# Kernel optimization log

Measured on AMD Instinct MI355X. Metric: run time of the kernel, lower is better.

Reference implementation:

```python
import jax, jax.numpy as jnp
import numpy as np

N, E, D, G, NTYPES = 50000, 400000, 64, 512, 64


def _bn(x, g, b):
    # BatchNorm1d in training mode: biased batch stats, eps=1e-5, affine g/b
    mu = x.mean(0)
    var = ((x - mu) ** 2).mean(0)
    return g * (x - mu) * jax.lax.rsqrt(var + 1e-5) + b


def _rotmat(a):
    t, p, q = a[0], a[1], a[2]
    ct, st = jnp.cos(t), jnp.sin(t)
    cp, sp = jnp.cos(p), jnp.sin(p)
    cq, sq = jnp.cos(q), jnp.sin(q)
    z = jnp.zeros(())
    o = jnp.ones(())
    Rt = jnp.array([[ct, -st, z], [st, ct, z], [z, z, o]])
    Rp = jnp.array([[cp, z, -sp], [z, o, z], [sp, z, cp]])
    Rq = jnp.array([[o, z, z], [z, cq, -sq], [z, sq, cq]])
    return Rt @ Rp @ Rq


def _egat(src, dst, nf, ef, Wnode, bnode, Wni, Wnj, Wfij, attn, H):
    # DGL EGATConv: edge feats from src/dst node + edge projections, edge-softmax attention over dst
    n = nf.shape[0]
    f_out = jax.nn.leaky_relu((nf @ Wni)[src] + (nf @ Wnj)[dst] + ef @ Wfij)  # [E, H*D]
    f_out = f_out.reshape(-1, H, D)
    e = (f_out * attn[None]).sum(-1)  # [E, H]
    emax = jax.ops.segment_max(e, dst, num_segments=n)
    ee = jnp.exp(e - emax[dst])
    a = ee / jax.ops.segment_sum(ee, dst, num_segments=n)[dst]
    hsrc = (nf @ Wnode + bnode).reshape(n, H, D)[src]
    h_out = jax.ops.segment_sum(hsrc * a[:, :, None], dst, num_segments=n)  # [N, H, D]
    return h_out, f_out


def _layer(src, dst, nh, eh, p, H, last):
    Wnode, bnode, Wni, Wnj, Wfij, attn, bnn_g, bnn_b, bne_g, bne_b, Wpn, bpn, Wpe, bpe = p
    hn, he = _egat(src, dst, nh, eh, Wnode, bnode, Wni, Wnj, Wfij, attn, H)
    if last:
        hn, he = hn.mean(1), he.mean(1)
    else:
        hn, he = hn.reshape(hn.shape[0], -1), he.reshape(he.shape[0], -1)
    hn = _bn(hn, bnn_g, bnn_b)
    he = _bn(he, bne_g, bne_b)
    return hn @ Wpn + bpn + nh, he @ Wpe + bpe + eh


def setup_inputs():
    key = jax.random.key(0)
    kit = iter(jax.random.split(key, 64))

    def rn(shape, s=0.05):
        return jax.random.normal(next(kit), shape, dtype=jnp.float32) * s

    inp = {}
    inp["ntype"] = jax.random.randint(next(kit), (N, 1), 0, NTYPES)
    inp["src"] = jax.random.randint(next(kit), (E,), 0, N)
    inp["dst"] = jax.random.randint(next(kit), (E,), 0, N)
    inp["graph_ids"] = jnp.sort(jax.random.randint(next(kit), (N,), 0, G))
    inp["angles_rot"] = rn((3,), 1.0)
    inp["angles_ref"] = rn((3,), 1.0)
    inp["efeats"] = rn((E, 3), 1.0)
    inp["emb_table"] = rn((NTYPES, D))
    inp["enc_W"] = rn((D, D)); inp["enc_b"] = jnp.zeros((D,))
    inp["ee_W1"] = rn((3, D)); inp["ee_b1"] = jnp.zeros((D,))
    inp["ee_W2"] = rn((D, D)); inp["ee_b2"] = jnp.zeros((D,))
    for nm in ["enc_bn1", "enc_bn2", "ee_bn1", "ee_bn2"]:
        inp[nm + "_g"] = jnp.ones((D,)); inp[nm + "_b"] = jnp.zeros((D,))
    for l, H in [(0, 2), (1, 1)]:
        p = "l%d_" % l
        inp[p + "Wnode"] = rn((D, H * D)); inp[p + "bnode"] = jnp.zeros((H * D,))
        inp[p + "Wni"] = rn((D, H * D)); inp[p + "Wnj"] = rn((D, H * D)); inp[p + "Wfij"] = rn((D, H * D))
        inp[p + "attn"] = rn((H, D))
        inp[p + "bnn_g"] = jnp.ones((H * D,)); inp[p + "bnn_b"] = jnp.zeros((H * D,))
        inp[p + "bne_g"] = jnp.ones((H * D,)); inp[p + "bne_b"] = jnp.zeros((H * D,))
        inp[p + "Wpn"] = rn((H * D, D)); inp[p + "bpn"] = jnp.zeros((D,))
        inp[p + "Wpe"] = rn((H * D, D)); inp[p + "bpe"] = jnp.zeros((D,))
    inp["dec_W"] = rn((4, D, D)); inp["dec_b"] = jnp.zeros((4, D))
    inp["dec_bn_g"] = jnp.ones((4, D)); inp["dec_bn_b"] = jnp.zeros((4, D))
    inp["dec_prelu"] = jnp.full((4,), 0.25, dtype=jnp.float32)
    inp["dec_Wout"] = rn((D, 1)); inp["dec_bout"] = jnp.zeros((1,))
    return inp


def reference(efeats, emb_table, enc_bn1_g, enc_bn1_b, enc_W, enc_b, enc_bn2_g, enc_bn2_b, ee_W1, ee_b1, ee_bn1_g, ee_bn1_b, ee_W2, ee_b2, ee_bn2_g, ee_bn2_b, l0_Wnode, l0_bnode, l0_Wni, l0_Wnj, l0_Wfij, l0_attn, l0_bnn_g, l0_bnn_b, l0_bne_g, l0_bne_b, l0_Wpn, l0_bpn, l0_Wpe, l0_bpe, l1_Wnode, l1_bnode, l1_Wni, l1_Wnj, l1_Wfij, l1_attn, l1_bnn_g, l1_bnn_b, l1_bne_g, l1_bne_b, l1_Wpn, l1_bpn, l1_Wpe, l1_bpe, dec_W, dec_b, dec_bn_g, dec_bn_b, dec_prelu, dec_Wout, dec_bout, ntype, src, dst, graph_ids, angles_rot, angles_ref):
    # node encoder: Embedding -> BN -> ReLU -> Linear -> BN -> ReLU
    nh = emb_table[ntype[:, 0]]
    nh = jax.nn.relu(_bn(nh, enc_bn1_g, enc_bn1_b))
    nh = jax.nn.relu(_bn(nh @ enc_W + enc_b, enc_bn2_g, enc_bn2_b))

    def edge_enc(f):
        h = jax.nn.relu(_bn(f @ ee_W1 + ee_b1, ee_bn1_g, ee_bn1_b))
        return jax.nn.relu(_bn(h @ ee_W2 + ee_b2, ee_bn2_g, ee_bn2_b))

    # rotation matrices built from sampled angles; torch.tensor([...]) detaches -> stop_gradient
    R_rot = jax.lax.stop_gradient(_rotmat(angles_rot))
    R_ref = -jax.lax.stop_gradient(_rotmat(angles_ref))
    eh = edge_enc(efeats @ R_rot) + edge_enc(efeats @ R_ref)

    p0 = (l0_Wnode, l0_bnode, l0_Wni, l0_Wnj, l0_Wfij, l0_attn, l0_bnn_g, l0_bnn_b, l0_bne_g, l0_bne_b, l0_Wpn, l0_bpn, l0_Wpe, l0_bpe)
    p1 = (l1_Wnode, l1_bnode, l1_Wni, l1_Wnj, l1_Wfij, l1_attn, l1_bnn_g, l1_bnn_b, l1_bne_g, l1_bne_b, l1_Wpn, l1_bpn, l1_Wpe, l1_bpe)
    nh, eh = _layer(src, dst, nh, eh, p0, 2, False)
    h1 = nh
    nh, eh = _layer(src, dst, nh, eh, p1, 1, True)
    h2 = nh

    h = nh
    for i in range(4):
        h = _bn(h @ dec_W[i] + dec_b[i], dec_bn_g[i], dec_bn_b[i])
        h = jnp.where(h >= 0.0, h, dec_prelu[i] * h)
    h = h @ dec_Wout + dec_bout
    # dgl.sum_nodes: per-graph sum over batched graphs
    return (h1, h2, jax.ops.segment_sum(h, graph_ids, num_segments=G))
```

## Files before the change

kernel.cpp:

```cpp
#include <hip/hip_runtime.h>
#include <math.h>

#define NN 50000
#define NE 400000
#define NG 512
#define EPS 1e-5f
#define NSLOT 256

typedef unsigned int u32;
typedef unsigned short u16;

typedef __attribute__((ext_vector_type(8))) short s16x8;
typedef __attribute__((ext_vector_type(4))) float f32x4;

__device__ __forceinline__ float b2f(u16 h) { return __uint_as_float(((u32)h) << 16); }
__device__ __forceinline__ u16 f2b(float f) {
    u32 x = __float_as_uint(f);
    u32 r = x + 0x7fffu + ((x >> 16) & 1u);
    return (u16)(r >> 16);
}
struct alignas(16) U16x8 { u16 s[8]; };
struct alignas(8) U16x4 { u16 s[4]; };
struct alignas(4) U16x2 { u16 s[2]; };

__device__ __forceinline__ void f4add(float4& a, const float4 b) {
    a.x += b.x; a.y += b.y; a.z += b.z; a.w += b.w;
}

__global__ void setup_kernel(const float* __restrict__ ang_rot, const float* __restrict__ ang_ref,
                             const float* __restrict__ W1, float* __restrict__ RWrot,
                             float* __restrict__ RWref) {
    int c = threadIdx.x;
    for (int which = 0; which < 2; ++which) {
        const float* a = which ? ang_ref : ang_rot;
        float t = a[0], p = a[1], q = a[2];
        float ct = cosf(t), st = sinf(t);
        float cp = cosf(p), sp = sinf(p);
        float cq = cosf(q), sq = sinf(q);
        float Rt[3][3] = {{ct, -st, 0.f}, {st, ct, 0.f}, {0.f, 0.f, 1.f}};
        float Rp[3][3] = {{cp, 0.f, -sp}, {0.f, 1.f, 0.f}, {sp, 0.f, cp}};
        float Rq[3][3] = {{1.f, 0.f, 0.f}, {0.f, cq, -sq}, {0.f, sq, cq}};
        float Rtp[3][3], R[3][3];
        for (int i = 0; i < 3; ++i)
            for (int j = 0; j < 3; ++j) {
                float s = 0.f;
                for (int k = 0; k < 3; ++k) s += Rt[i][k] * Rp[k][j];
                Rtp[i][j] = s;
            }
        for (int i = 0; i < 3; ++i)
            for (int j = 0; j < 3; ++j) {
                float s = 0.f;
                for (int k = 0; k < 3; ++k) s += Rtp[i][k] * Rq[k][j];
                R[i][j] = s;
            }
        float sgn = which ? -1.f : 1.f;
        float* RW = which ? RWref : RWrot;
        if (c < 64) {
            for (int j = 0; j < 3; ++j) {
                float s = 0.f;
                for (int m = 0; m < 3; ++m) s += sgn * R[j][m] * W1[m * 64 + c];
                RW[j * 64 + c] = s;
            }
        }
    }
}

#define NWT 17
struct WtJobs {
    const float* W[NWT];
    u16* WT[NWT];
    int K[NWT];
    int C[NWT];
};
__global__ __launch_bounds__(256) void wt_all_kernel(WtJobs jobs) {
    int job = blockIdx.x >> 5;
    int idx = ((blockIdx.x & 31) << 8) + threadIdx.x;
    int K = jobs.K[job], C = jobs.C[job];
    if (idx >= K * C) return;
    int k = idx / C, c = idx - k * C;
    jobs.WT[job][c * K + k] = f2b(jobs.W[job][idx]);
}

__global__ __launch_bounds__(256) void hist_kernel(const int* __restrict__ dst, int E,
                                                   int* __restrict__ deg) {
    int e = blockIdx.x * 256 + threadIdx.x;
    if (e < E) atomicAdd(&deg[dst[e]], 1);
}

__global__ __launch_bounds__(256) void scan_part_kernel(const int* __restrict__ deg,
                                                        int* __restrict__ bsum, int n) {
    int i = blockIdx.x * 256 + threadIdx.x;
    int v = (i < n) ? deg[i] : 0;
#pragma unroll
    for (int off = 1; off < 64; off <<= 1) v += __shfl_xor(v, off, 64);
    __shared__ int ws[4];
    if ((threadIdx.x & 63) == 0) ws[threadIdx.x >> 6] = v;
    __syncthreads();
    if (threadIdx.x == 0) bsum[blockIdx.x] = ws[0] + ws[1] + ws[2] + ws[3];
}

__global__ __launch_bounds__(256) void scan_top_kernel(int* __restrict__ bsum, int nb,
                                                       int* __restrict__ rowptr, int n,
                                                       int total) {
    __shared__ int s[256];
    int tid = threadIdx.x;
    s[tid] = (tid < nb) ? bsum[tid] : 0;
    __syncthreads();
    for (int off = 1; off < 256; off <<= 1) {
        int v = (tid >= off) ? s[tid - off] : 0;
        __syncthreads();
        s[tid] += v;
        __syncthreads();
    }
    if (tid < nb) bsum[tid] = (tid == 0) ? 0 : s[tid - 1];
    if (tid == 0) rowptr[n] = total;
}

__global__ __launch_bounds__(256) void scan_fill_kernel(const int* __restrict__ deg,
                                                        const int* __restrict__ bsum,
                                                        int* __restrict__ rowptr,
                                                        int* __restrict__ curs, int n) {
    __shared__ int s[256];
    int tid = threadIdx.x;
    int i = blockIdx.x * 256 + tid;
    int v = (i < n) ? deg[i] : 0;
    s[tid] = v;
    __syncthreads();
    for (int off = 1; off < 256; off <<= 1) {
        int t = (tid >= off) ? s[tid - off] : 0;
        __syncthreads();
        s[tid] += t;
        __syncthreads();
    }
    if (i < n) {
        int excl = s[tid] - v + bsum[blockIdx.x];
        rowptr[i] = excl;
        curs[i] = excl;
    }
}

__global__ __launch_bounds__(256) void fill_kernel(const int* __restrict__ src,
                                                   const int* __restrict__ dst,
                                                   const float* __restrict__ ef, int E,
                                                   int* __restrict__ curs,
                                                   int* __restrict__ esrc,
                                                   int* __restrict__ dsts,
                                                   float* __restrict__ efp) {
    int e = blockIdx.x * 256 + threadIdx.x;
    if (e >= E) return;
    int d = dst[e];
    int pos = atomicAdd(&curs[d], 1);
    esrc[pos] = src[e];
    dsts[pos] = d;
    efp[(long)pos * 3 + 0] = ef[(long)e * 3 + 0];
    efp[(long)pos * 3 + 1] = ef[(long)e * 3 + 1];
    efp[(long)pos * 3 + 2] = ef[(long)e * 3 + 2];
}

__global__ __launch_bounds__(256) void gather_emb_kernel(const int* __restrict__ ntype,
                                                         const float* __restrict__ emb,
                                                         u16* __restrict__ out, int n) {
    long i = (long)blockIdx.x * 256 + threadIdx.x;
    long e = i >> 3;
    if (e >= n) return;
    int c0 = (int)(i & 7) * 8;
    int t = ntype[e];
    float4 a = *(const float4*)&emb[(long)t * 64 + c0];
    float4 b = *(const float4*)&emb[(long)t * 64 + c0 + 4];
    U16x8 o;
    o.s[0] = f2b(a.x); o.s[1] = f2b(a.y); o.s[2] = f2b(a.z); o.s[3] = f2b(a.w);
    o.s[4] = f2b(b.x); o.s[5] = f2b(b.y); o.s[6] = f2b(b.z); o.s[7] = f2b(b.w);
    *(U16x8*)&out[e * 64 + c0] = o;
}

__global__ __launch_bounds__(256) void efstats_kernel(const float* __restrict__ ef, int E,
                                                      float* __restrict__ raw) {
    int tid = threadIdx.x;
    float a[9];
#pragma unroll
    for (int j = 0; j < 9; ++j) a[j] = 0.f;
    for (long e = (long)blockIdx.x * 256 + tid; e < E; e += (long)gridDim.x * 256) {
        float f0 = ef[e * 3 + 0], f1 = ef[e * 3 + 1], f2 = ef[e * 3 + 2];
        a[0] += f0; a[1] += f1; a[2] += f2;
        a[3] += f0 * f0; a[4] += f1 * f1; a[5] += f2 * f2;
        a[6] += f0 * f1; a[7] += f0 * f2; a[8] += f1 * f2;
    }
#pragma unroll
    for (int off = 1; off < 64; off <<= 1)
#pragma unroll
        for (int j = 0; j < 9; ++j) a[j] += __shfl_xor(a[j], off, 64);
    __shared__ float sred[4][9];
    int wv = tid >> 6, ln = tid & 63;
    if (ln == 0)
#pragma unroll
        for (int j = 0; j < 9; ++j) sred[wv][j] = a[j];
    __syncthreads();
    if (tid < 9) {
        float v = sred[0][tid] + sred[1][tid] + sred[2][tid] + sred[3][tid];
        atomicAdd(&raw[(size_t)(blockIdx.x & (NSLOT - 1)) * 16 + tid], v);
    }
}

__global__ void ee_stats_kernel(const float* __restrict__ efraw, const float* __restrict__ RWrot,
                                const float* __restrict__ RWref, const float* __restrict__ b1,
                                float* __restrict__ S_rot, float* __restrict__ S_ref, int E) {
    __shared__ float m[9];
    int t = threadIdx.x;
    if (t < 9) {
        float s = 0.f;
        for (int r = 0; r < NSLOT; ++r) s += efraw[r * 16 + t];
        m[t] = s;
    }
    __syncthreads();
    int br = t >> 6, c = t & 63;
    const float* RW = br ? RWref : RWrot;
    float* S = br ? S_ref : S_rot;
    float w0 = RW[c], w1 = RW[64 + c], w2 = RW[128 + c];
    float bb = b1[c];
    float mw = m[0] * w0 + m[1] * w1 + m[2] * w2;
    float sum = mw + (float)E * bb;
    float quad = m[3] * w0 * w0 + m[4] * w1 * w1 + m[5] * w2 * w2 +
                 2.f * (m[6] * w0 * w1 + m[7] * w0 * w2 + m[8] * w1 * w2);
    float ss = quad + 2.f * bb * mw + (float)E * bb * bb;
    S[c] = sum;
    S[64 + c] = ss;
}

template <int COLS>
__global__ __launch_bounds__(256) void colstats_kernel(const u16* __restrict__ xv, int rows,
                                                       float* __restrict__ raw) {
    constexpr int TPR = COLS / 8;
    constexpr int RPB = 256 / TPR;
    __shared__ float4 sA[256], sB[256], sC[256], sD[256];
    int tid = threadIdx.x;
    int c8 = tid % TPR;
    int rl = tid / TPR;
    float s[8], q[8];
#pragma unroll
    for (int j = 0; j < 8; ++j) { s[j] = 0.f; q[j] = 0.f; }
    const long stride = (long)gridDim.x * RPB;
    for (long r = (long)blockIdx.x * RPB + rl; r < rows; r += stride) {
        U16x8 t = *(const U16x8*)&xv[r * COLS + c8 * 8];
#pragma unroll
        for (int j = 0; j < 8; ++j) {
            float v = b2f(t.s[j]);
            s[j] += v;
            q[j] += v * v;
        }
    }
    sA[tid] = make_float4(s[0], s[1], s[2], s[3]);
    sB[tid] = make_float4(s[4], s[5], s[6], s[7]);
    sC[tid] = make_float4(q[0], q[1], q[2], q[3]);
    sD[tid] = make_float4(q[4], q[5], q[6], q[7]);
    __syncthreads();
    for (int off = 128; off >= TPR; off >>= 1) {
        if (tid < off) {
            f4add(sA[tid], sA[tid + off]); f4add(sB[tid], sB[tid + off]);
            f4add(sC[tid], sC[tid + off]); f4add(sD[tid], sD[tid + off]);
        }
        __syncthreads();
    }
    if (tid < TPR) {
        float* slot = raw + (size_t)(blockIdx.x & (NSLOT - 1)) * 256;
        int c = tid * 8;
        float4 a = sA[tid], b = sB[tid], cq = sC[tid], d = sD[tid];
        atomicAdd(&slot[c + 0], a.x); atomicAdd(&slot[c + 1], a.y);
        atomicAdd(&slot[c + 2], a.z); atomicAdd(&slot[c + 3], a.w);
        atomicAdd(&slot[c + 4], b.x); atomicAdd(&slot[c + 5], b.y);
        atomicAdd(&slot[c + 6], b.z); atomicAdd(&slot[c + 7], b.w);
        atomicAdd(&slot[COLS + c + 0], cq.x); atomicAdd(&slot[COLS + c + 1], cq.y);
        atomicAdd(&slot[COLS + c + 2], cq.z); atomicAdd(&slot[COLS + c + 3], cq.w);
        atomicAdd(&slot[COLS + c + 4], d.x); atomicAdd(&slot[COLS + c + 5], d.y);
        atomicAdd(&slot[COLS + c + 6], d.z); atomicAdd(&slot[COLS + c + 7], d.w);
    }
}

__global__ __launch_bounds__(256) void finalize_stats_kernel(const float* __restrict__ raw,
                                                             float* __restrict__ stats, int n) {
    int i = threadIdx.x;
    if (i >= n) return;
    float s = 0.f;
    for (int r = 0; r < NSLOT; ++r) s += raw[r * 256 + i];
    stats[i] = s;
}

__global__ __launch_bounds__(256) void bn_act_kernel(const u16* __restrict__ x,
                                                     u16* __restrict__ y, long rows, int cols,
                                                     const float* __restrict__ acc,
                                                     const float* __restrict__ g,
                                                     const float* __restrict__ b,
                                                     float inv_rows) {
    long i = (long)blockIdx.x * 256 + threadIdx.x;
    long total8 = rows * (long)cols / 8;
    if (i >= total8) return;
    long base = i * 8;
    int c0 = (int)(base % cols);
    U16x8 xv = *(const U16x8*)&x[base];
    U16x8 o;
#pragma unroll
    for (int j = 0; j < 8; ++j) {
        int c = c0 + j;
        float mu = acc[c] * inv_rows;
        float var = acc[cols + c] * inv_rows - mu * mu;
        float al = g[c] * rsqrtf(fmaxf(var, 0.f) + EPS);
        float be = b[c] - mu * al;
        o.s[j] = f2b(fmaxf(al * b2f(xv.s[j]) + be, 0.f));
    }
    *(U16x8*)&y[base] = o;
}


template <int K, int COLS, bool XBF, bool RBF, bool OBF, bool SOUT>
__global__ __launch_bounds__(256) void mfma_mm_kernel(
    const void* __restrict__ Xv, const u16* __restrict__ WT, const float* __restrict__ bias,
    const void* __restrict__ resv, void* __restrict__ Yv, int rows, int preop,
    const float* __restrict__ stats, const float* __restrict__ g, const float* __restrict__ b,
    float inv_rows, const float* __restrict__ prelu, int prelu_idx, float* __restrict__ raw) {
    constexpr int NCT = COLS / 16;
    constexpr int NKK = K / 32;
    __shared__ float al[K], be[K];
    __shared__ float ssum[SOUT ? COLS : 1], ssq[SOUT ? COLS : 1];
    const int tid = threadIdx.x;
    if (preop) {
        for (int k = tid; k < K; k += 256) {
            float mu = stats[k] * inv_rows;
            float var = stats[K + k] * inv_rows - mu * mu;
            float a = g[k] * rsqrtf(fmaxf(var, 0.f) + EPS);
            al[k] = a;
            be[k] = b[k] - mu * a;
        }
    }
    if (SOUT) {
        for (int i = tid; i < COLS; i += 256) { ssum[i] = 0.f; ssq[i] = 0.f; }
    }
    __syncthreads();
    const int lane = tid & 63, wv = tid >> 6;
    const int q = lane >> 4, rr = lane & 15;
    const long r0 = ((long)blockIdx.x * 4 + wv) * 16;
    const bool act = r0 < rows;
    const float pa = (preop == 3) ? prelu[prelu_idx] : 0.f;
    s16x8 afr[NKK];
    if (act) {
#pragma unroll
        for (int kk = 0; kk < NKK; ++kk) {
            float v[8];
            if (XBF) {
                U16x8 t = *(const U16x8*)((const u16*)Xv + (r0 + rr) * K + kk * 32 + q * 8);
#pragma unroll
                for (int j = 0; j < 8; ++j) v[j] = b2f(t.s[j]);
            } else {
                const float* xp = (const float*)Xv + (r0 + rr) * K + kk * 32 + q * 8;
                float4 t0 = *(const float4*)xp;
                float4 t1 = *(const float4*)(xp + 4);
                v[0] = t0.x; v[1] = t0.y; v[2] = t0.z; v[3] = t0.w;
                v[4] = t1.x; v[5] = t1.y; v[6] = t1.z; v[7] = t1.w;
            }
            union { u16 u[8]; s16x8 s; } o;
#pragma unroll
            for (int j = 0; j < 8; ++j) {
                float xx = v[j];
                if (preop) {
                    int k = kk * 32 + q * 8 + j;
                    xx = al[k] * xx + be[k];
                    if (preop == 2) xx = fmaxf(xx, 0.f);
                    else if (preop == 3) xx = (xx >= 0.f) ? xx : pa * xx;
                }
                o.u[j] = f2b(xx);
            }
            afr[kk] = o.s;
        }
#pragma unroll
        for (int ct = 0; ct < NCT; ++ct) {
            f32x4 acc = (f32x4){0.f, 0.f, 0.f, 0.f};
#pragma unroll
            for (int kk = 0; kk < NKK; ++kk) {
                s16x8 bfr = *(const s16x8*)&WT[(size_t)(ct * 16 + rr) * K + kk * 32 + q * 8];
                acc = __builtin_amdgcn_mfma_f32_16x16x32_bf16(afr[kk], bfr, acc, 0, 0, 0);
            }
            int col = ct * 16 + rr;
            float bb = bias ? bias[col] : 0.f;
            float fs = 0.f, fq = 0.f;
#pragma unroll
            for (int r = 0; r < 4; ++r) {
                long orr = r0 + q * 4 + r;
                float vv = acc[r] + bb;
                if (resv) {
                    if (RBF) vv += b2f(((const u16*)resv)[orr * COLS + col]);
                    else vv += ((const float*)resv)[orr * COLS + col];
                }
                if (OBF) ((u16*)Yv)[orr * COLS + col] = f2b(vv);
                else ((float*)Yv)[orr * COLS + col] = vv;
                if (SOUT) { fs += vv; fq += vv * vv; }
            }
            if (SOUT) {
                fs += __shfl_xor(fs, 16, 64); fs += __shfl_xor(fs, 32, 64);
                fq += __shfl_xor(fq, 16, 64); fq += __shfl_xor(fq, 32, 64);
                if (q == 0) {
                    atomicAdd(&ssum[col], fs);
                    atomicAdd(&ssq[col], fq);
                }
            }
        }
    }
    if (SOUT) {
        __syncthreads();
        float* slot = raw + (size_t)(blockIdx.x & (NSLOT - 1)) * 256;
        for (int i = tid; i < COLS; i += 256) {
            atomicAdd(&slot[i], ssum[i]);
            atomicAdd(&slot[COLS + i], ssq[i]);
        }
    }
}

template <int COLS, bool XBF>
__global__ __launch_bounds__(256) void mfma_mm3_kernel(
    const void* __restrict__ Xv, const u16* __restrict__ WT0, const u16* __restrict__ WT1,
    const u16* __restrict__ WT2, const float* __restrict__ bias2, u16* __restrict__ Y0,
    u16* __restrict__ Y1, u16* __restrict__ Y2, int rows) {
    constexpr int NCT = COLS / 16;
    const int tid = threadIdx.x;
    const int lane = tid & 63, wv = tid >> 6;
    const int q = lane >> 4, rr = lane & 15;
    const long r0 = ((long)blockIdx.x * 4 + wv) * 16;
    if (r0 >= rows) return;
    s16x8 afr[2];
#pragma unroll
    for (int kk = 0; kk < 2; ++kk) {
        if (XBF) {
            afr[kk] = *(const s16x8*)((const u16*)Xv + (r0 + rr) * 64 + kk * 32 + q * 8);
        } else {
            const float* xp = (const float*)Xv + (r0 + rr) * 64 + kk * 32 + q * 8;
            float4 t0 = *(const float4*)xp;
            float4 t1 = *(const float4*)(xp + 4);
            union { u16 u[8]; s16x8 s; } o;
            o.u[0] = f2b(t0.x); o.u[1] = f2b(t0.y); o.u[2] = f2b(t0.z); o.u[3] = f2b(t0.w);
            o.u[4] = f2b(t1.x); o.u[5] = f2b(t1.y); o.u[6] = f2b(t1.z); o.u[7] = f2b(t1.w);
            afr[kk] = o.s;
        }
    }
    const u16* wts[3] = {WT0, WT1, WT2};
    u16* ys[3] = {Y0, Y1, Y2};
#pragma unroll
    for (int m = 0; m < 3; ++m) {
#pragma unroll
        for (int ct = 0; ct < NCT; ++ct) {
            f32x4 acc = (f32x4){0.f, 0.f, 0.f, 0.f};
#pragma unroll
            for (int kk = 0; kk < 2; ++kk) {
                s16x8 bfr = *(const s16x8*)&wts[m][(size_t)(ct * 16 + rr) * 64 + kk * 32 + q * 8];
                acc = __builtin_amdgcn_mfma_f32_16x16x32_bf16(afr[kk], bfr, acc, 0, 0, 0);
            }
            int col = ct * 16 + rr;
            float bb = (m == 2) ? bias2[col] : 0.f;
#pragma unroll
            for (int r = 0; r < 4; ++r) {
                long orr = r0 + q * 4 + r;
                ys[m][orr * COLS + col] = f2b(acc[r] + bb);
            }
        }
    }
}

template <bool STORE>
__global__ __launch_bounds__(256) void mfma_ee2_kernel(
    const float* __restrict__ efp, const float* __restrict__ RWrot,
    const float* __restrict__ RWref, const float* __restrict__ b1v, const u16* __restrict__ W2T,
    const float* __restrict__ b2, const float* __restrict__ S1r, const float* __restrict__ S1f,
    const float* __restrict__ S2r, const float* __restrict__ S2f, const float* __restrict__ g1,
    const float* __restrict__ bn1b, const float* __restrict__ g2, const float* __restrict__ bn2b,
    u16* __restrict__ EH, int E, float inv_rows, float* __restrict__ rawA,
    float* __restrict__ rawB) {
    constexpr int ESTR = 72;
    __shared__ float rws[2][192];
    __shared__ float al1[2][64], be1[2][64];
    __shared__ float al2[2][64], be2[2][64];
    __shared__ float ssum[2][64], ssq[2][64];
    __shared__ u16 ets[STORE ? 64 * ESTR : 1];
    const int tid = threadIdx.x;
    if (tid < 192) {
        rws[0][tid] = RWrot[tid];
        rws[1][tid] = RWref[tid];
    }
    if (tid < 128) {
        int br = tid >> 6, k = tid & 63;
        const float* S1 = br ? S1f : S1r;
        float mu = S1[k] * inv_rows;
        float var = S1[64 + k] * inv_rows - mu * mu;
        float a = g1[k] * rsqrtf(fmaxf(var, 0.f) + EPS);
        al1[br][k] = a;
        be1[br][k] = bn1b[k] - mu * a + a * b1v[k];
        if (STORE) {
            const float* S2 = br ? S2f : S2r;
            mu = S2[k] * inv_rows;
            var = S2[64 + k] * inv_rows - mu * mu;
            a = g2[k] * rsqrtf(fmaxf(var, 0.f) + EPS);
            al2[br][k] = a;
            be2[br][k] = bn2b[k] - mu * a + a * b2[k];
        } else {
            ssum[br][k] = 0.f;
            ssq[br][k] = 0.f;
        }
    }
    __syncthreads();
    const int lane = tid & 63, wv = tid >> 6;
    const int q = lane >> 4, rr = lane & 15;
    const long r0 = ((long)blockIdx.x * 4 + wv) * 16;
    const long ar = r0 + rr;
    float e0 = efp[ar * 3], e1 = efp[ar * 3 + 1], e2 = efp[ar * 3 + 2];
    float v0[4][4];
#pragma unroll
    for (int br = 0; br < 2; ++br) {
        s16x8 afr[2];
#pragma unroll
        for (int kk = 0; kk < 2; ++kk) {
            union { u16 u[8]; s16x8 v; } t;
#pragma unroll
            for (int j = 0; j < 8; ++j) {
                int k = kk * 32 + q * 8 + j;
                float tv = e0 * rws[br][k] + e1 * rws[br][64 + k] + e2 * rws[br][128 + k];
                t.u[j] = f2b(fmaxf(al1[br][k] * tv + be1[br][k], 0.f));
            }
            afr[kk] = t.v;
        }
#pragma unroll
        for (int ct = 0; ct < 4; ++ct) {
            f32x4 acc = (f32x4){0.f, 0.f, 0.f, 0.f};
#pragma unroll
            for (int kk = 0; kk < 2; ++kk) {
                s16x8 bfr = *(const s16x8*)&W2T[(size_t)(ct * 16 + rr) * 64 + kk * 32 + q * 8];
                acc = __builtin_amdgcn_mfma_f32_16x16x32_bf16(afr[kk], bfr, acc, 0, 0, 0);
            }
            int col = ct * 16 + rr;
            if (STORE) {
#pragma unroll
                for (int r = 0; r < 4; ++r) {
                    float v = fmaxf(al2[br][col] * acc[r] + be2[br][col], 0.f);
                    if (br == 0) {
                        v0[ct][r] = v;
                    } else {
                        ets[(wv * 16 + q * 4 + r) * ESTR + col] = f2b(v0[ct][r] + v);
                    }
                }
            } else {
                float bb = b2[col];
                float s = 0.f, qq = 0.f;
#pragma unroll
                for (int r = 0; r < 4; ++r) {
                    float v = acc[r] + bb;
                    s += v;
                    qq += v * v;
                }
                s += __shfl_xor(s, 16, 64); s += __shfl_xor(s, 32, 64);
                qq += __shfl_xor(qq, 16, 64); qq += __shfl_xor(qq, 32, 64);
                if (q == 0) {
                    atomicAdd(&ssum[br][col], s);
                    atomicAdd(&ssq[br][col], qq);
                }
            }
        }
    }
    __syncthreads();
    if (STORE) {
        const long rb = (long)blockIdx.x * 64;
        for (int i = tid; i < 64 * 8; i += 256) {
            int row = i >> 3, c8 = i & 7;
            U16x8 v = *(const U16x8*)&ets[row * ESTR + c8 * 8];
            *(U16x8*)&EH[(rb + row) * 64 + c8 * 8] = v;
        }
    } else {
        if (tid < 128) {
            int br = tid >> 6, k = tid & 63;
            float* slot = (br ? rawB : rawA) + (size_t)(blockIdx.x & (NSLOT - 1)) * 256;
            atomicAdd(&slot[k], ssum[br][k]);
            atomicAdd(&slot[64 + k], ssq[br][k]);
        }
    }
}

template <int COLS, bool WRITE_F, bool SOUT>
__global__ __launch_bounds__(256) void mfma_egat_kernel(
    const u16* __restrict__ EH, const u16* __restrict__ WT, const u16* __restrict__ NI,
    const u16* __restrict__ NJ, const int* __restrict__ srcs, const int* __restrict__ dsts,
    const float* __restrict__ attn, u16* __restrict__ Fout, float* __restrict__ eatt, int E,
    float* __restrict__ raw) {
    constexpr int H = COLS / 64;
    constexpr int NCT = COLS / 16;
    constexpr int FSTR = COLS + 8;
    __shared__ float ssum[SOUT ? COLS : 1];
    __shared__ float ssq[SOUT ? COLS : 1];
    __shared__ u16 fts[WRITE_F ? 64 * FSTR : 1];
    const int tid = threadIdx.x;
    if (SOUT) {
        for (int i = tid; i < COLS; i += 256) { ssum[i] = 0.f; ssq[i] = 0.f; }
        __syncthreads();
    }
    const int lane = tid & 63, wv = tid >> 6;
    const int q = lane >> 4, rr = lane & 15;
    const long r0 = ((long)blockIdx.x * 4 + wv) * 16;
    s16x8 afr[2];
#pragma unroll
    for (int kk = 0; kk < 2; ++kk)
        afr[kk] = *(const s16x8*)&EH[(r0 + rr) * 64 + kk * 32 + q * 8];
    int sidx[4], didx[4];
#pragma unroll
    for (int r = 0; r < 4; ++r) {
        long orr = r0 + q * 4 + r;
        sidx[r] = srcs[orr];
        didx[r] = dsts[orr];
    }
    f32x4 acc[NCT];
#pragma unroll
    for (int ct = 0; ct < NCT; ++ct) {
        acc[ct] = (f32x4){0.f, 0.f, 0.f, 0.f};
#pragma unroll
        for (int kk = 0; kk < 2; ++kk) {
            s16x8 bfr = *(const s16x8*)&WT[(size_t)(ct * 16 + rr) * 64 + kk * 32 + q * 8];
            acc[ct] = __builtin_amdgcn_mfma_f32_16x16x32_bf16(afr[kk], bfr, acc[ct], 0, 0, 0);
        }
    }
    float part[H][4];
#pragma unroll
    for (int h = 0; h < H; ++h)
#pragma unroll
        for (int r = 0; r < 4; ++r) part[h][r] = 0.f;
#pragma unroll
    for (int ct = 0; ct < NCT; ++ct) {
        int col = ct * 16 + rr;
        float av = attn[col];
        const int h = (H == 2) ? (ct >> 2) : 0;
        float fs = 0.f, fq = 0.f;
#pragma unroll
        for (int r = 0; r < 4; ++r) {
            float f = acc[ct][r] + b2f(NI[(size_t)sidx[r] * COLS + col]) +
                      b2f(NJ[(size_t)didx[r] * COLS + col]);
            f = (f >= 0.f) ? f : 0.01f * f;
            if (WRITE_F) fts[(wv * 16 + q * 4 + r) * FSTR + col] = f2b(f);
            part[h][r] += f * av;
            if (SOUT) { fs += f; fq += f * f; }
        }
        if (SOUT) {
            fs += __shfl_xor(fs, 16, 64); fs += __shfl_xor(fs, 32, 64);
            fq += __shfl_xor(fq, 16, 64); fq += __shfl_xor(fq, 32, 64);
            if (q == 0) {
                atomicAdd(&ssum[col], fs);
                atomicAdd(&ssq[col], fq);
            }
        }
    }
#pragma unroll
    for (int h = 0; h < H; ++h)
#pragma unroll
        for (int r = 0; r < 4; ++r) {
            float p = part[h][r];
            p += __shfl_xor(p, 1, 64);
            p += __shfl_xor(p, 2, 64);
            p += __shfl_xor(p, 4, 64);
            p += __shfl_xor(p, 8, 64);
            part[h][r] = p;
        }
    if (rr == 0) {
#pragma unroll
        for (int r = 0; r < 4; ++r) {
            long pos = r0 + q * 4 + r;
            if (H == 2) {
                eatt[pos * 2 + 0] = part[0][r];
                eatt[pos * 2 + 1] = part[1][r];
            } else {
                eatt[pos] = part[0][r];
            }
        }
    }
    if (WRITE_F) {
        __syncthreads();
        const long rb = (long)blockIdx.x * 64;
        constexpr int CH = COLS / 8;
        for (int i = tid; i < 64 * CH; i += 256) {
            int row = i / CH, c8 = i % CH;
            U16x8 v = *(const U16x8*)&fts[row * FSTR + c8 * 8];
            *(U16x8*)&Fout[(rb + row) * COLS + c8 * 8] = v;
        }
    }
    if (SOUT) {
        __syncthreads();
        float* slot = raw + (size_t)(blockIdx.x & (NSLOT - 1)) * 256;
        for (int i = tid; i < COLS; i += 256) {
            atomicAdd(&slot[i], ssum[i]);
            atomicAdd(&slot[COLS + i], ssq[i]);
        }
    }
}

__global__ __launch_bounds__(256) void mfma_pe_kernel(
    const u16* __restrict__ X, const u16* __restrict__ WT, const float* __restrict__ bias,
    u16* __restrict__ EHio, int E, const float* __restrict__ stats, const float* __restrict__ g,
    const float* __restrict__ b, float inv_rows) {
    __shared__ float al[128], be[128];
    const int tid = threadIdx.x;
    if (tid < 128) {
        float mu = stats[tid] * inv_rows;
        float var = stats[128 + tid] * inv_rows - mu * mu;
        float a = g[tid] * rsqrtf(fmaxf(var, 0.f) + EPS);
        al[tid] = a;
        be[tid] = b[tid] - mu * a;
    }
    __syncthreads();
    const int lane = tid & 63, wv = tid >> 6;
    const int q = lane >> 4, rr = lane & 15;
    const long r0 = ((long)blockIdx.x * 4 + wv) * 16;
    s16x8 afr[4];
#pragma unroll
    for (int kk = 0; kk < 4; ++kk) {
        U16x8 t = *(const U16x8*)&X[(r0 + rr) * 128 + kk * 32 + q * 8];
        union { u16 u[8]; s16x8 v; } o;
#pragma unroll
        for (int j = 0; j < 8; ++j) {
            int k = kk * 32 + q * 8 + j;
            o.u[j] = f2b(al[k] * b2f(t.s[j]) + be[k]);
        }
        afr[kk] = o.v;
    }
#pragma unroll
    for (int ct = 0; ct < 4; ++ct) {
        f32x4 acc = (f32x4){0.f, 0.f, 0.f, 0.f};
#pragma unroll
        for (int kk = 0; kk < 4; ++kk) {
            s16x8 bfr = *(const s16x8*)&WT[(size_t)(ct * 16 + rr) * 128 + kk * 32 + q * 8];
            acc = __builtin_amdgcn_mfma_f32_16x16x32_bf16(afr[kk], bfr, acc, 0, 0, 0);
        }
        int col = ct * 16 + rr;
        float bb = bias[col];
#pragma unroll
        for (int r = 0; r < 4; ++r) {
            long orr = r0 + q * 4 + r;
            float v = acc[r] + bb + b2f(EHio[orr * 64 + col]);
            EHio[orr * 64 + col] = f2b(v);
        }
    }
}

template <int COLS, bool SOUT>
__global__ __launch_bounds__(256) void csr_aggregate_kernel(
    const int* __restrict__ rowptr, const int* __restrict__ esrc,
    const float* __restrict__ eatt, const u16* __restrict__ nodeh, float* __restrict__ hout,
    int n, float* __restrict__ raw) {
    constexpr int H = COLS / 64;
    constexpr int TPN = COLS / 2;
    constexpr int NPB = 256 / TPN;
    __shared__ float ssum[SOUT ? COLS : 1];
    __shared__ float ssq[SOUT ? COLS : 1];
    int tid = threadIdx.x;
    if (SOUT) {
        for (int i = tid; i < COLS; i += 256) { ssum[i] = 0.f; ssq[i] = 0.f; }
        __syncthreads();
    }
    int node = blockIdx.x * NPB + tid / TPN;
    bool act = node < n;
    int c = (tid % TPN) * 2;
    float a0 = 0.f, a1 = 0.f;
    if (act) {
        int h = (H == 2) ? (c >> 6) : 0;
        int p0 = rowptr[node], p1 = rowptr[node + 1];
        float m = -INFINITY, s = 0.f;
        for (int p = p0; p < p1; ++p) {
            float v = eatt[(long)p * H + h];
            float mn = fmaxf(m, v);
            s = s * expf(m - mn) + expf(v - mn);
            m = mn;
        }
        float inv = (s > 0.f) ? 1.f / s : 0.f;
        for (int p = p0; p < p1; ++p) {
            float w = expf(eatt[(long)p * H + h] - m) * inv;
            U16x2 v = *(const U16x2*)&nodeh[(long)esrc[p] * COLS + c];
            a0 += b2f(v.s[0]) * w;
            a1 += b2f(v.s[1]) * w;
        }
        *(float2*)&hout[(long)node * COLS + c] = make_float2(a0, a1);
    }
    if (SOUT) {
        if (act) {
            atomicAdd(&ssum[c], a0);
            atomicAdd(&ssum[c + 1], a1);
            atomicAdd(&ssq[c], a0 * a0);
            atomicAdd(&ssq[c + 1], a1 * a1);
        }
        __syncthreads();
        float* slot = raw + (size_t)(blockIdx.x & (NSLOT - 1)) * 256;
        for (int i = tid; i < COLS; i += 256) {
            atomicAdd(&slot[i], ssum[i]);
            atomicAdd(&slot[COLS + i], ssq[i]);
        }
    }
}

__global__ __launch_bounds__(256) void decoder_out_kernel(
    const u16* __restrict__ t3, const float* __restrict__ stats, const float* __restrict__ g,
    const float* __restrict__ b, const float* __restrict__ prelu, const float* __restrict__ Wout,
    const float* __restrict__ bout, const int* __restrict__ gid, float* __restrict__ pool,
    int rows, float inv_rows) {
    int tid = threadIdx.x;
    long r = (long)blockIdx.x * 4 + (tid >> 6);
    if (r >= rows) return;
    int k = tid & 63;
    float mu = stats[k] * inv_rows;
    float var = stats[64 + k] * inv_rows - mu * mu;
    float al = g[k] * rsqrtf(fmaxf(var, 0.f) + EPS);
    float be = b[k] - mu * al;
    float a = prelu[3];
    float v = al * b2f(t3[r * 64 + k]) + be;
    v = (v >= 0.f) ? v : a * v;
    v *= Wout[k];
#pragma unroll
    for (int off = 1; off < 64; off <<= 1) v += __shfl_xor(v, off, 64);
    if (k == 0) atomicAdd(&pool[gid[r]], v + bout[0]);
}

extern "C" void kernel_launch(void* const* d_in, const int* in_sizes, int n_in, void* d_out,
                              int out_size, void* d_ws, size_t ws_size, hipStream_t stream) {
    if (n_in < 57) return;
    const int* ntype = (const int*)d_in[0];
    const int* src = (const int*)d_in[1];
    const int* dst = (const int*)d_in[2];
    const int* gid = (const int*)d_in[3];
    const float* ang_rot = (const float*)d_in[4];
    const float* ang_ref = (const float*)d_in[5];
    const float* efeats = (const float*)d_in[6];
    const float* emb = (const float*)d_in[7];
    const float* enc_W = (const float*)d_in[8];
    const float* enc_b = (const float*)d_in[9];
    const float* ee_W1 = (const float*)d_in[10];
    const float* ee_b1 = (const float*)d_in[11];
    const float* ee_W2 = (const float*)d_in[12];
    const float* ee_b2 = (const float*)d_in[13];
    const float* enc_bn1_g = (const float*)d_in[14];
    const float* enc_bn1_b = (const float*)d_in[15];
    const float* enc_bn2_g = (const float*)d_in[16];
    const float* enc_bn2_b = (const float*)d_in[17];
    const float* ee_bn1_g = (const float*)d_in[18];
    const float* ee_bn1_b = (const float*)d_in[19];
    const float* ee_bn2_g = (const float*)d_in[20];
    const float* ee_bn2_b = (const float*)d_in[21];
    const float* l0_Wnode = (const float*)d_in[22];
    const float* l0_bnode = (const float*)d_in[23];
    const float* l0_Wni = (const float*)d_in[24];
    const float* l0_Wnj = (const float*)d_in[25];
    const float* l0_Wfij = (const float*)d_in[26];
    const float* l0_attn = (const float*)d_in[27];
    const float* l0_bnn_g = (const float*)d_in[28];
    const float* l0_bnn_b = (const float*)d_in[29];
    const float* l0_bne_g = (const float*)d_in[30];
    const float* l0_bne_b = (const float*)d_in[31];
    const float* l0_Wpn = (const float*)d_in[32];
    const float* l0_bpn = (const float*)d_in[33];
    const float* l0_Wpe = (const float*)d_in[34];
    const float* l0_bpe = (const float*)d_in[35];
    const float* l1_Wnode = (const float*)d_in[36];
    const float* l1_bnode = (const float*)d_in[37];
    const float* l1_Wni = (const float*)d_in[38];
    const float* l1_Wnj = (const float*)d_in[39];
    const float* l1_Wfij = (const float*)d_in[40];
    const float* l1_attn = (const float*)d_in[41];
    const float* l1_bnn_g = (const float*)d_in[42];
    const float* l1_bnn_b = (const float*)d_in[43];
    const float* l1_Wpn = (const float*)d_in[46];
    const float* l1_bpn = (const float*)d_in[47];
    const float* dec_W = (const float*)d_in[50];
    const float* dec_b = (const float*)d_in[51];
    const float* dec_bn_g = (const float*)d_in[52];
    const float* dec_bn_b = (const float*)d_in[53];
    const float* dec_prelu = (const float*)d_in[54];
    const float* dec_Wout = (const float*)d_in[55];
    const float* dec_bout = (const float*)d_in[56];

    float* out = (float*)d_out;
    float* H1 = out;
    float* H2 = out + (long)NN * 64;
    float* POOL = out + (long)NN * 128;

    char* base = (char*)d_ws;
    size_t off = 0;
    auto alloc = [&](size_t bytes) -> void* {
        off = (off + 255) & ~(size_t)255;
        void* p = base + off;
        off += bytes;
        return p;
    };
    u16* EH = (u16*)alloc((size_t)NE * 64 * 2);
    u16* F128 = (u16*)alloc((size_t)NE * 128 * 2);
    float* EATT = (float*)alloc((size_t)NE * 2 * 4);
    u16* NX = (u16*)alloc((size_t)NN * 64 * 2);
    u16* NI = (u16*)alloc((size_t)NN * 128 * 2);
    u16* NJ = (u16*)alloc((size_t)NN * 128 * 2);
    u16* NHH = (u16*)alloc((size_t)NN * 128 * 2);
    float* HOUT0 = (float*)alloc((size_t)NN * 128 * 4);
    float* HOUT1 = (float*)alloc((size_t)NN * 64 * 4);
    int* ROWPTR = (int*)alloc((size_t)(NN + 1) * 4);
    int* CURS = (int*)alloc((size_t)NN * 4);
    int* ESRC = (int*)alloc((size_t)NE * 4);
    int* DSTS = (int*)alloc((size_t)NE * 4);
    float* EFP = (float*)alloc((size_t)NE * 3 * 4);
    int* BSUM = (int*)alloc((size_t)256 * 4);
    float* RWrot = (float*)alloc(256 * 4);
    float* RWref = (float*)alloc(256 * 4);
    u16* EncWT = (u16*)alloc(4096 * 2);
    u16* W2T = (u16*)alloc(4096 * 2);
    u16* Wni0T = (u16*)alloc(8192 * 2);
    u16* Wnj0T = (u16*)alloc(8192 * 2);
    u16* Wnd0T = (u16*)alloc(8192 * 2);
    u16* WfijT0 = (u16*)alloc(8192 * 2);
    u16* Wpn0T = (u16*)alloc(8192 * 2);
    u16* WpeT = (u16*)alloc(8192 * 2);
    u16* Wni1T = (u16*)alloc(4096 * 2);
    u16* Wnj1T = (u16*)alloc(4096 * 2);
    u16* Wnd1T = (u16*)alloc(4096 * 2);
    u16* WfijT1 = (u16*)alloc(4096 * 2);
    u16* Wpn1T = (u16*)alloc(4096 * 2);
    u16* DecT0 = (u16*)alloc(4096 * 2);
    u16* DecT1 = (u16*)alloc(4096 * 2);
    u16* DecT2 = (u16*)alloc(4096 * 2);
    u16* DecT3 = (u16*)alloc(4096 * 2);
    float* STATS = (float*)alloc((size_t)13 * 256 * 4);
    char* zstart = base + ((off + 255) & ~(size_t)255);
    int* DEG = (int*)alloc((size_t)NN * 4);
    float* STATS_RAW = (float*)alloc((size_t)13 * NSLOT * 256 * 4);
    float* RAWEF = (float*)alloc((size_t)NSLOT * 16 * 4);
    char* zend = base + off;
    if (ws_size < off) return;

    u16* NX0 = F128;
    u16* NT = F128 + (size_t)NN * 64;
    u16* DT0 = NI;
    u16* DT1 = NJ;

    auto RAW = [&](int idx) { return STATS_RAW + (size_t)idx * NSLOT * 256; };
    float* S_enc1 = STATS + 0 * 256;
    float* S_enc2 = STATS + 1 * 256;
    float* S_ee1r = STATS + 2 * 256;
    float* S_ee2r = STATS + 3 * 256;
    float* S_ee1f = STATS + 4 * 256;
    float* S_ee2f = STATS + 5 * 256;
    float* S_bnn0 = STATS + 6 * 256;
    float* S_bne0 = STATS + 7 * 256;
    float* S_bnn1 = STATS + 8 * 256;
    float* S_d0 = STATS + 9 * 256;
    float* S_d1 = STATS + 10 * 256;
    float* S_d2 = STATS + 11 * 256;
    float* S_d3 = STATS + 12 * 256;

    const float invN = 1.f / (float)NN;
    const float invE = 1.f / (float)NE;
    const int GS = 640;
    const int MFB = NE / 64;
    const int NNB = (NN + 63) / 64;
    const int NB = (NN + 255) / 256;

    hipMemsetAsync(zstart, 0, (size_t)(zend - zstart), stream);
    hipMemsetAsync(POOL, 0, (size_t)NG * 4, stream);

    setup_kernel<<<1, 64, 0, stream>>>(ang_rot, ang_ref, ee_W1, RWrot, RWref);
    {
        WtJobs j;
        const float* Ws[NWT] = {enc_W,  ee_W2,  l0_Wni, l0_Wnj, l0_Wnode, l0_Wfij,
                                l0_Wpn, l0_Wpe, l1_Wni, l1_Wnj, l1_Wnode, l1_Wfij,
                                l1_Wpn, dec_W,  dec_W + 4096, dec_W + 8192, dec_W + 12288};
        u16* Ts[NWT] = {EncWT, W2T, Wni0T, Wnj0T, Wnd0T, WfijT0, Wpn0T, WpeT, Wni1T,
                        Wnj1T, Wnd1T, WfijT1, Wpn1T, DecT0, DecT1, DecT2, DecT3};
        int Ks[NWT] = {64, 64, 64, 64, 64, 64, 128, 128, 64, 64, 64, 64, 64, 64, 64, 64, 64};
        int Cs[NWT] = {64, 64, 128, 128, 128, 128, 64, 64, 64, 64, 64, 64, 64, 64, 64, 64, 64};
        for (int i = 0; i < NWT; ++i) { j.W[i] = Ws[i]; j.WT[i] = Ts[i]; j.K[i] = Ks[i]; j.C[i] = Cs[i]; }
        wt_all_kernel<<<NWT * 32, 256, 0, stream>>>(j);
    }

    hist_kernel<<<(NE + 255) / 256, 256, 0, stream>>>(dst, NE, DEG);
    scan_part_kernel<<<NB, 256, 0, stream>>>(DEG, BSUM, NN);
    scan_top_kernel<<<1, 256, 0, stream>>>(BSUM, NB, ROWPTR, NN, NE);
    scan_fill_kernel<<<NB, 256, 0, stream>>>(DEG, BSUM, ROWPTR, CURS, NN);
    fill_kernel<<<(NE + 255) / 256, 256, 0, stream>>>(src, dst, efeats, NE, CURS, ESRC, DSTS,
                                                      EFP);

    gather_emb_kernel<<<(NN * 8 + 255) / 256, 256, 0, stream>>>(ntype, emb, NX0, NN);
    colstats_kernel<64><<<GS, 256, 0, stream>>>(NX0, NN, RAW(0));
    finalize_stats_kernel<<<1, 256, 0, stream>>>(RAW(0), S_enc1, 128);
    mfma_mm_kernel<64, 64, true, false, true, true><<<NNB, 256, 0, stream>>>(
        NX0, EncWT, enc_b, nullptr, NT, NN, 2, S_enc1, enc_bn1_g, enc_bn1_b, invN, nullptr, 0,
        RAW(1));
    finalize_stats_kernel<<<1, 256, 0, stream>>>(RAW(1), S_enc2, 128);
    bn_act_kernel<<<(NN * 8 + 255) / 256, 256, 0, stream>>>(NT, NX, NN, 64, S_enc2, enc_bn2_g,
                                                            enc_bn2_b, invN);

    efstats_kernel<<<256, 256, 0, stream>>>(efeats, NE, RAWEF);
    ee_stats_kernel<<<1, 128, 0, stream>>>(RAWEF, RWrot, RWref, ee_b1, S_ee1r, S_ee1f, NE);
    mfma_ee2_kernel<false><<<MFB, 256, 0, stream>>>(
        EFP, RWrot, RWref, ee_b1, W2T, ee_b2, S_ee1r, S_ee1f, nullptr, nullptr, ee_bn1_g,
        ee_bn1_b, nullptr, nullptr, nullptr, NE, invE, RAW(3), RAW(5));
    finalize_stats_kernel<<<1, 256, 0, stream>>>(RAW(3), S_ee2r, 128);
    finalize_stats_kernel<<<1, 256, 0, stream>>>(RAW(5), S_ee2f, 128);
    mfma_ee2_kernel<true><<<MFB, 256, 0, stream>>>(
        EFP, RWrot, RWref, ee_b1, W2T, ee_b2, S_ee1r, S_ee1f, S_ee2r, S_ee2f, ee_bn1_g, ee_bn1_b,
        ee_bn2_g, ee_bn2_b, EH, NE, invE, nullptr, nullptr);

    mfma_mm3_kernel<128, true><<<NNB, 256, 0, stream>>>(NX, Wni0T, Wnj0T, Wnd0T, l0_bnode, NI,
                                                        NJ, NHH, NN);
    mfma_egat_kernel<128, true, true><<<MFB, 256, 0, stream>>>(
        EH, WfijT0, NI, NJ, ESRC, DSTS, l0_attn, F128, EATT, NE, RAW(7));
    finalize_stats_kernel<<<1, 256, 0, stream>>>(RAW(7), S_bne0, 256);
    csr_aggregate_kernel<128, true><<<(NN + 3) / 4, 256, 0, stream>>>(ROWPTR, ESRC, EATT, NHH,
                                                                      HOUT0, NN, RAW(6));
    finalize_stats_kernel<<<1, 256, 0, stream>>>(RAW(6), S_bnn0, 256);
    mfma_mm_kernel<128, 64, false, true, false, false><<<NNB, 256, 0, stream>>>(
        HOUT0, Wpn0T, l0_bpn, NX, H1, NN, 1, S_bnn0, l0_bnn_g, l0_bnn_b, invN, nullptr, 0,
        nullptr);
    mfma_pe_kernel<<<MFB, 256, 0, stream>>>(F128, WpeT, l0_bpe, EH, NE, S_bne0, l0_bne_g,
                                            l0_bne_b, invE);

    mfma_mm3_kernel<64, false><<<NNB, 256, 0, stream>>>(H1, Wni1T, Wnj1T, Wnd1T, l1_bnode, NI,
                                                        NJ, NHH, NN);
    mfma_egat_kernel<64, false, false><<<MFB, 256, 0, stream>>>(
        EH, WfijT1, NI, NJ, ESRC, DSTS, l1_attn, nullptr, EATT, NE, nullptr);
    csr_aggregate_kernel<64, true><<<(NN + 7) / 8, 256, 0, stream>>>(ROWPTR, ESRC, EATT, NHH,
                                                                     HOUT1, NN, RAW(8));
    finalize_stats_kernel<<<1, 256, 0, stream>>>(RAW(8), S_bnn1, 128);
    mfma_mm_kernel<64, 64, false, false, false, false><<<NNB, 256, 0, stream>>>(
        HOUT1, Wpn1T, l1_bpn, H1, H2, NN, 1, S_bnn1, l1_bnn_g, l1_bnn_b, invN, nullptr, 0,
        nullptr);

    mfma_mm_kernel<64, 64, false, false, true, true><<<NNB, 256, 0, stream>>>(
        H2, DecT0, dec_b, nullptr, DT0, NN, 0, nullptr, nullptr, nullptr, 0.f, nullptr, 0,
        RAW(9));
    finalize_stats_kernel<<<1, 256, 0, stream>>>(RAW(9), S_d0, 128);
    mfma_mm_kernel<64, 64, true, false, true, true><<<NNB, 256, 0, stream>>>(
        DT0, DecT1, dec_b + 64, nullptr, DT1, NN, 3, S_d0, dec_bn_g, dec_bn_b, invN, dec_prelu,
        0, RAW(10));
    finalize_stats_kernel<<<1, 256, 0, stream>>>(RAW(10), S_d1, 128);
    mfma_mm_kernel<64, 64, true, false, true, true><<<NNB, 256, 0, stream>>>(
        DT1, DecT2, dec_b + 128, nullptr, DT0, NN, 3, S_d1, dec_bn_g + 64, dec_bn_b + 64, invN,
        dec_prelu, 1, RAW(11));
    finalize_stats_kernel<<<1, 256, 0, stream>>>(RAW(11), S_d2, 128);
    mfma_mm_kernel<64, 64, true, false, true, true><<<NNB, 256, 0, stream>>>(
        DT0, DecT3, dec_b + 192, nullptr, DT1, NN, 3, S_d2, dec_bn_g + 128, dec_bn_b + 128,
        invN, dec_prelu, 2, RAW(12));
    finalize_stats_kernel<<<1, 256, 0, stream>>>(RAW(12), S_d3, 128);
    decoder_out_kernel<<<(NN + 3) / 4, 256, 0, stream>>>(DT1, S_d3, dec_bn_g + 192,
                                                         dec_bn_b + 192, dec_prelu, dec_Wout,
                                                         dec_bout, gid, POOL, NN, invN);
}
```

Before: 878.0 us.

## Stage MFMA results in LDS to vectorize edge gathers and residual updates

The edge EGAT kernel now writes the raw MFMA accumulators to shared memory first. It then does a second pass in which each thread handles 8 contiguous columns per row, doing 16-byte gathers of the NI/NJ node rows plus leaky-ReLU, the attention dot product (reduced per row through shared atomics), and the BN statistics. Before, each lane issued scalar 2-byte gathers. The edge projection kernel likewise stages its output in LDS and does the residual read-modify-write with 16-byte vector accesses. This adds an extra LDS round trip, an unconditional shared buffer and shared atomics per row, and it rounds the matmul result to bf16 before adding the node terms, which slightly changes numerics.

```diff
diff --git a/kernel.cpp b/kernel.cpp
--- a/kernel.cpp
+++ b/kernel.cpp
@@ -586,13 +586,16 @@
     constexpr int H = COLS / 64;
     constexpr int NCT = COLS / 16;
     constexpr int FSTR = COLS + 8;
+    constexpr int CH = COLS / 8;
+    constexpr int RPG = 256 / CH;
+    __shared__ u16 fts[64 * FSTR];
+    __shared__ float rowsum[64 * 2];
     __shared__ float ssum[SOUT ? COLS : 1];
     __shared__ float ssq[SOUT ? COLS : 1];
-    __shared__ u16 fts[WRITE_F ? 64 * FSTR : 1];
     const int tid = threadIdx.x;
+    if (tid < 128) rowsum[tid] = 0.f;
     if (SOUT) {
         for (int i = tid; i < COLS; i += 256) { ssum[i] = 0.f; ssq[i] = 0.f; }
-        __syncthreads();
     }
     const int lane = tid & 63, wv = tid >> 6;
     const int q = lane >> 4, rr = lane & 15;
@@ -601,87 +604,73 @@
 #pragma unroll
     for (int kk = 0; kk < 2; ++kk)
         afr[kk] = *(const s16x8*)&EH[(r0 + rr) * 64 + kk * 32 + q * 8];
-    int sidx[4], didx[4];
-#pragma unroll
-    for (int r = 0; r < 4; ++r) {
-        long orr = r0 + q * 4 + r;
-        sidx[r] = srcs[orr];
-        didx[r] = dsts[orr];
-    }
-    f32x4 acc[NCT];
 #pragma unroll
     for (int ct = 0; ct < NCT; ++ct) {
-        acc[ct] = (f32x4){0.f, 0.f, 0.f, 0.f};
+        f32x4 acc = (f32x4){0.f, 0.f, 0.f, 0.f};
 #pragma unroll
         for (int kk = 0; kk < 2; ++kk) {
             s16x8 bfr = *(const s16x8*)&WT[(size_t)(ct * 16 + rr) * 64 + kk * 32 + q * 8];
-            acc[ct] = __builtin_amdgcn_mfma_f32_16x16x32_bf16(afr[kk], bfr, acc[ct], 0, 0, 0);
-        }
-    }
-    float part[H][4];
-#pragma unroll
-    for (int h = 0; h < H; ++h)
-#pragma unroll
-        for (int r = 0; r < 4; ++r) part[h][r] = 0.f;
-#pragma unroll
-    for (int ct = 0; ct < NCT; ++ct) {
+            acc = __builtin_amdgcn_mfma_f32_16x16x32_bf16(afr[kk], bfr, acc, 0, 0, 0);
+        }
         int col = ct * 16 + rr;
-        float av = attn[col];
-        const int h = (H == 2) ? (ct >> 2) : 0;
-        float fs = 0.f, fq = 0.f;
-#pragma unroll
-        for (int r = 0; r < 4; ++r) {
-            float f = acc[ct][r] + b2f(NI[(size_t)sidx[r] * COLS + col]) +
-                      b2f(NJ[(size_t)didx[r] * COLS + col]);
+#pragma unroll
+        for (int r = 0; r < 4; ++r)
+            fts[(wv * 16 + q * 4 + r) * FSTR + col] = f2b(acc[r]);
+    }
+    __syncthreads();
+    const long rb = (long)blockIdx.x * 64;
+    const int c8 = tid % CH;
+    const int rloc = tid / CH;
+    float av[8];
+    {
+        float4 a0 = *(const float4*)&attn[c8 * 8];
+        float4 a1 = *(const float4*)&attn[c8 * 8 + 4];
+        av[0] = a0.x; av[1] = a0.y; av[2] = a0.z; av[3] = a0.w;
+        av[4] = a1.x; av[5] = a1.y; av[6] = a1.z; av[7] = a1.w;
+    }
+    const int h = (H == 2) ? (c8 >> 3) : 0;
+    float fs[8], fq[8];
+#pragma unroll
+    for (int j = 0; j < 8; ++j) { fs[j] = 0.f; fq[j] = 0.f; }
+#pragma unroll
+    for (int g = 0; g < 64 / RPG; ++g) {
+        int row = g * RPG + rloc;
+        int s = srcs[rb + row];
+        int d = dsts[rb + row];
+        U16x8 ni = *(const U16x8*)&NI[(size_t)s * COLS + c8 * 8];
+        U16x8 nj = *(const U16x8*)&NJ[(size_t)d * COLS + c8 * 8];
+        U16x8 ft = *(const U16x8*)&fts[row * FSTR + c8 * 8];
+        float part = 0.f;
+        U16x8 fo;
+#pragma unroll
+        for (int j = 0; j < 8; ++j) {
+            float f = b2f(ft.s[j]) + b2f(ni.s[j]) + b2f(nj.s[j]);
             f = (f >= 0.f) ? f : 0.01f * f;
-            if (WRITE_F) fts[(wv * 16 + q * 4 + r) * FSTR + col] = f2b(f);
-            part[h][r] += f * av;
-            if (SOUT) { fs += f; fq += f * f; }
-        }
-        if (SOUT) {
-            fs += __shfl_xor(fs, 16, 64); fs += __shfl_xor(fs, 32, 64);
-            fq += __shfl_xor(fq, 16, 64); fq += __shfl_xor(fq, 32, 64);
-            if (q == 0) {
-                atomicAdd(&ssum[col], fs);
-                atomicAdd(&ssq[col], fq);
-            }
-        }
-    }
-#pragma unroll
-    for (int h = 0; h < H; ++h)
-#pragma unroll
-        for (int r = 0; r < 4; ++r) {
-            float p = part[h][r];
-            p += __shfl_xor(p, 1, 64);
-            p += __shfl_xor(p, 2, 64);
-            p += __shfl_xor(p, 4, 64);
-            p += __shfl_xor(p, 8, 64);
-            part[h][r] = p;
-        }
-    if (rr == 0) {
-#pragma unroll
-        for (int r = 0; r < 4; ++r) {
-            long pos = r0 + q * 4 + r;
-            if (H == 2) {
-                eatt[pos * 2 + 0] = part[0][r];
-                eatt[pos * 2 + 1] = part[1][r];
-            } else {
-                eatt[pos] = part[0][r];
-            }
-        }
-    }
-    if (WRITE_F) {
-        __syncthreads();
-        const long rb = (long)blockIdx.x * 64;
-        constexpr int CH = COLS / 8;
-        for (int i = tid; i < 64 * CH; i += 256) {
-            int row = i / CH, c8 = i % CH;
-            U16x8 v = *(const U16x8*)&fts[row * FSTR + c8 * 8];
-            *(U16x8*)&Fout[(rb + row) * COLS + c8 * 8] = v;
-        }
+            fo.s[j] = f2b(f);
+            part += f * av[j];
+            if (SOUT) { fs[j] += f; fq[j] += f * f; }
+        }
+        if (WRITE_F) *(U16x8*)&Fout[(rb + row) * COLS + c8 * 8] = fo;
+        atomicAdd(&rowsum[row * 2 + h], part);
     }
     if (SOUT) {
-        __syncthreads();
+#pragma unroll
+        for (int j = 0; j < 8; ++j) {
+            atomicAdd(&ssum[c8 * 8 + j], fs[j]);
+            atomicAdd(&ssq[c8 * 8 + j], fq[j]);
+        }
+    }
+    __syncthreads();
+    if (tid < 64) {
+        long pos = rb + tid;
+        if (H == 2) {
+            eatt[pos * 2 + 0] = rowsum[tid * 2 + 0];
+            eatt[pos * 2 + 1] = rowsum[tid * 2 + 1];
+        } else {
+            eatt[pos] = rowsum[tid * 2 + 0];
+        }
+    }
+    if (SOUT) {
         float* slot = raw + (size_t)(blockIdx.x & (NSLOT - 1)) * 256;
         for (int i = tid; i < COLS; i += 256) {
             atomicAdd(&slot[i], ssum[i]);
@@ -694,7 +683,9 @@
     const u16* __restrict__ X, const u16* __restrict__ WT, const float* __restrict__ bias,
     u16* __restrict__ EHio, int E, const float* __restrict__ stats, const float* __restrict__ g,
     const float* __restrict__ b, float inv_rows) {
+    constexpr int ESTR = 72;
     __shared__ float al[128], be[128];
+    __shared__ u16 ets[64 * ESTR];
     const int tid = threadIdx.x;
     if (tid < 128) {
         float mu = stats[tid] * inv_rows;
@@ -730,11 +721,21 @@
         int col = ct * 16 + rr;
         float bb = bias[col];
 #pragma unroll
-        for (int r = 0; r < 4; ++r) {
-            long orr = r0 + q * 4 + r;
-            float v = acc[r] + bb + b2f(EHio[orr * 64 + col]);
-            EHio[orr * 64 + col] = f2b(v);
-        }
+        for (int r = 0; r < 4; ++r)
+            ets[(wv * 16 + q * 4 + r) * ESTR + col] = f2b(acc[r] + bb);
+    }
+    __syncthreads();
+    const long rb = (long)blockIdx.x * 64;
+#pragma unroll
+    for (int g = 0; g < 2; ++g) {
+        int i = g * 256 + tid;
+        int row = i >> 3, c8 = i & 7;
+        U16x8 st = *(const U16x8*)&ets[row * ESTR + c8 * 8];
+        U16x8 old = *(const U16x8*)&EHio[(rb + row) * 64 + c8 * 8];
+        U16x8 o;
+#pragma unroll
+        for (int j = 0; j < 8; ++j) o.s[j] = f2b(b2f(st.s[j]) + b2f(old.s[j]));
+        *(U16x8*)&EHio[(rb + row) * 64 + c8 * 8] = o;
     }
 }
 
```

New measurement: 985.6 us. 1.12x slower.
